# Kernel tuning notes

Hardware: AMD Instinct MI355X
Metric: run time of the kernel (lower is better)

## Reference

```python
import jax, jax.numpy as jnp
import numpy as np

U = I = 4096; E = 128; K = 4; D = E // K; R = 3; B = 512; L = 100
LAMB = 0.5; L2NORM = 1e-4; EPS = 1e-8


def _l2norm(x, axis):
    n = jnp.sqrt(jnp.sum(x * x, axis=axis, keepdims=True))
    return x / jnp.maximum(n, 1e-12)


def setup_inputs() -> dict:
    key = jax.random.key(0)
    ks = jax.random.split(key, 16)
    def adj(k, shape, p=0.01):
        return jax.random.bernoulli(k, p, shape).astype(jnp.float32)
    relation_mats = adj(ks[0], (R, U, I))
    item_graphs = adj(ks[1], (R, I, I))
    train_matrix = relation_mats[0]
    inp = {
        "user": jax.random.randint(ks[2], (B, 1), 0, U),
        "item": jax.random.randint(ks[3], (B, L), 0, I),
        "user_embedding": jax.random.normal(ks[4], (U, E), jnp.float32) * 0.1,
        "item_embedding": jax.random.normal(ks[5], (I, E), jnp.float32) * 0.1,
        "mgnn_weight": jax.random.normal(ks[6], (R,), jnp.float32),
        "item_behaviour_W": jax.random.normal(ks[7], (R, E, E), jnp.float32) * 0.05,
        "item_propagate_W": jax.random.normal(ks[8], (R, E, E), jnp.float32) * 0.05,
        "W": jax.random.normal(ks[9], (E, E), jnp.float32) * 0.05,
        "W_K": jax.random.normal(ks[10], (K, D, E), jnp.float32) * 0.05,
        "B_K": jax.random.normal(ks[11], (K, D), jnp.float32) * 0.05,
        "train_matrix": train_matrix,
        "relation_mats": relation_mats,
        "item_graphs": item_graphs,
        "item_graph_degree": item_graphs.sum(axis=2, keepdims=True),  # [R,I,1]
        "user_behaviour_degree": relation_mats.sum(axis=2).T,  # [U,R]
    }
    return inp


def reference(user, item, user_embedding, item_embedding, mgnn_weight,
              item_behaviour_W, item_propagate_W, W, W_K, B_K,
              train_matrix, relation_mats, item_graphs, item_graph_degree,
              user_behaviour_degree):
    # behaviour weighting: [U,R]
    total_weight = user_behaviour_degree @ mgnn_weight[:, None]  # [U,1]
    ubw = user_behaviour_degree * mgnn_weight[None, :] / (total_weight + EPS)

    # K-head projections (relation-independent; original recomputes identically per relation)
    s_i = _l2norm(jax.nn.relu(jnp.einsum('kde,ie->kdi', W_K, item_embedding) + B_K[..., None]), axis=1)  # [K,D,I]
    s_u0 = _l2norm(jax.nn.relu(jnp.einsum('kde,ue->kdu', W_K, user_embedding) + B_K[..., None]), axis=1)  # [K,D,U]
    s_u0 = jnp.transpose(s_u0, (2, 0, 1))  # [U,K,D]

    ue_blocks = user_embedding.reshape(U, K, D)
    logits = jnp.einsum('ukd,kdi->kui', ue_blocks, s_i)  # [K,U,I]
    r = jax.nn.softmax(logits, axis=0)  # exp / sum over K heads

    user_feature = jnp.zeros((U, E), user_embedding.dtype)
    score2 = jnp.zeros((B, L), user_embedding.dtype)
    for i in range(R):
        rel = relation_mats[i]  # [U,I]
        # item-item propagation
        tip = ((item_graphs[i] @ item_embedding) / (item_graph_degree[i] + EPS)) @ item_propagate_W[i]  # [I,E]
        tmp_item_emb = tip[item]  # [B,L,E]
        # attention-weighted user-item propagation per head
        s_u = s_u0 + jnp.einsum('kui,kdi->ukd', r * rel[None], s_i)  # [U,K,D]
        tun = _l2norm(s_u, axis=2).reshape(U, E)  # tmp_user_neighbour
        tuinp = (rel @ tip) / (user_behaviour_degree[:, i:i + 1] + EPS)  # [U,E]
        user_feature = user_feature + ubw[:, i:i + 1] * tun
        proj = tuinp @ item_behaviour_W[i]  # [U,E]
        score2 = score2 + jnp.sum(proj[user[:, 0]][:, None, :] * tmp_item_emb, axis=2)
    score2 = score2 / R

    item_feature = (train_matrix.T @ user_embedding) @ W  # [I,E]
    user_feature = user_feature @ W  # [U,E]

    uf = user_feature[user[:, 0]][:, None, :]  # [B,1,E]
    itf = item_feature[item]  # [B,L,E]
    score1 = jnp.sum(uf * itf, axis=2)  # [B,L]
    scores = score1 + LAMB * score2
    L2_loss = L2NORM * (L * jnp.sum(uf ** 2) + jnp.sum(itf ** 2))
    return scores, L2_loss
```

## Files before the change

### kernel.cpp

```cpp
#include <hip/hip_runtime.h>

#define NU 4096
#define NI 4096
#define NR 3
#define NB 512
#define NL 100
#define FEPS 1e-8f

typedef float nf4 __attribute__((ext_vector_type(4)));

#define WS_SI    0
#define WS_EMBW  524288
#define WS_TIP   2097152
#define WS_UEW   3670016
#define WS_ITEMF 4194304
#define WS_PROJ  4915200
#define WS_UF    5111808
#define WS_UF2P  5177344
#define WS_ITF2P 5177856
#define WS_BMT   5190656

__global__ void k_prep(const float* __restrict__ iemb, const float* __restrict__ ipW,
                       const float* __restrict__ uemb, const float* __restrict__ Wm,
                       const float* __restrict__ WK, const float* __restrict__ BK,
                       const float* __restrict__ tm,
                       float* __restrict__ embW, float* __restrict__ uew,
                       float* __restrict__ si, unsigned long long* __restrict__ bmT) {
  int t = threadIdx.x;
  int bid = blockIdx.x;
  if (bid < 4096) {
    __shared__ unsigned char nib[4][256];
    const nf4* r4 = (const nf4*)(tm + (size_t)bid * NI);
#pragma unroll
    for (int q = 0; q < 4; ++q) {
      nf4 v = __builtin_nontemporal_load(&r4[q * 256 + t]);
      unsigned m = 0;
      if (v.x != 0.f) m |= 1u;
      if (v.y != 0.f) m |= 2u;
      if (v.z != 0.f) m |= 4u;
      if (v.w != 0.f) m |= 8u;
      nib[q][t] = (unsigned char)m;
    }
    __syncthreads();
    if (t < 64) {
      unsigned long long mm = 0;
#pragma unroll
      for (int j = 0; j < 16; ++j) {
        int e = t * 16 + j;
        mm |= (unsigned long long)nib[e >> 8][e & 255] << (4 * j);
      }
      bmT[(size_t)t * NU + bid] = mm;
    }
  } else if (bid < 5120) {
    __shared__ __align__(16) float shbuf[2048];
    int lb = bid - 4096;
    int batch = lb >> 8, rb = lb & 255;
    const float* in;
    const float* Wp;
    float* out;
    if (batch < 3) {
      in = iemb;
      Wp = ipW + (size_t)batch * 16384;
      out = embW + (size_t)batch * NI * 128;
    } else {
      in = uemb; Wp = Wm; out = uew;
    }
    const float4* in4 = (const float4*)(in + (size_t)rb * 2048);
    for (int c = t; c < 512; c += 256) ((float4*)shbuf)[c] = in4[c];
    __syncthreads();
    int c = t & 127, g = t >> 7;
    float acc[8];
#pragma unroll
    for (int rr = 0; rr < 8; ++rr) acc[rr] = 0.f;
    for (int e = 0; e < 128; ++e) {
      float wv = Wp[e * 128 + c];
#pragma unroll
      for (int rr = 0; rr < 8; ++rr) acc[rr] += shbuf[(g * 8 + rr) * 128 + e] * wv;
    }
#pragma unroll
    for (int rr = 0; rr < 8; ++rr) out[((size_t)rb * 16 + g * 8 + rr) * 128 + c] = acc[rr];
  } else {
    __shared__ __align__(16) float embs2[256];
    int tl = t & 127, half = t >> 7;
    int item = (bid - 5120) * 2 + half;
    float* embs = embs2 + half * 128;
    if (tl < 32) ((float4*)embs)[tl] = ((const float4*)(iemb + (size_t)item * 128))[tl];
    __syncthreads();
    float acc = BK[tl];
    const float4* wk4 = (const float4*)(WK + (size_t)tl * 128);
    const float4* e4 = (const float4*)embs;
#pragma unroll 8
    for (int cc = 0; cc < 32; ++cc) {
      float4 w = wk4[cc], v = e4[cc];
      acc += w.x * v.x + w.y * v.y + w.z * v.z + w.w * v.w;
    }
    acc = fmaxf(acc, 0.f);
    float sq = acc * acc;
#pragma unroll
    for (int m = 1; m <= 16; m <<= 1) sq += __shfl_xor(sq, m);
    si[(size_t)item * 128 + tl] = acc / fmaxf(sqrtf(sq), 1e-12f);
  }
}

__global__ void k_tipf(const float* __restrict__ G, const float* __restrict__ deg,
                       const float* __restrict__ embW,
                       const unsigned long long* __restrict__ bmT,
                       const float* __restrict__ uew,
                       float* __restrict__ tip, float* __restrict__ itemf) {
  int t = threadIdx.x;
  int bid = blockIdx.x;
  if (bid < 12288) {
    int r = bid >> 12;
    const nf4* row4 = (const nf4*)(G + (size_t)bid * NI);
    __shared__ int nz[512];
    __shared__ int cnt;
    __shared__ float4 red[8][32];
    if (t == 0) cnt = 0;
    __syncthreads();
#pragma unroll
    for (int c = 0; c < 4; ++c) {
      int idx4 = c * 256 + t;
      nf4 v = __builtin_nontemporal_load(&row4[idx4]);
      int j0 = idx4 << 2;
      if (v.x != 0.f) nz[atomicAdd(&cnt, 1)] = j0;
      if (v.y != 0.f) nz[atomicAdd(&cnt, 1)] = j0 + 1;
      if (v.z != 0.f) nz[atomicAdd(&cnt, 1)] = j0 + 2;
      if (v.w != 0.f) nz[atomicAdd(&cnt, 1)] = j0 + 3;
    }
    __syncthreads();
    int n = min(cnt, 512);
    int g = t >> 5, f = t & 31;
    float4 acc = {0.f, 0.f, 0.f, 0.f};
    const float4* e4 = (const float4*)(embW + (size_t)r * NI * 128);
    for (int p = g; p < n; p += 8) {
      float4 v = e4[(size_t)nz[p] * 32 + f];
      acc.x += v.x; acc.y += v.y; acc.z += v.z; acc.w += v.w;
    }
    red[g][f] = acc;
    __syncthreads();
    if (t < 32) {
      float4 s = red[0][t];
#pragma unroll
      for (int q = 1; q < 8; ++q) {
        float4 v = red[q][t];
        s.x += v.x; s.y += v.y; s.z += v.z; s.w += v.w;
      }
      float inv = 1.f / (deg[bid] + FEPS);
      s.x *= inv; s.y *= inv; s.z *= inv; s.w *= inv;
      ((float4*)(tip + (size_t)bid * 128))[t] = s;
    }
  } else {
    int i = bid - 12288;
    int ct = i >> 6;
    unsigned long long bitm = 1ull << (i & 63);
    __shared__ int lst[192];
    __shared__ int cnt2;
    __shared__ float red2[3][128];
    if (t == 0) cnt2 = 0;
    __syncthreads();
    const unsigned long long* col = bmT + (size_t)ct * NU;
#pragma unroll
    for (int cc = 0; cc < 16; ++cc) {
      unsigned long long m = col[cc * 256 + t];
      if (m & bitm) lst[atomicAdd(&cnt2, 1)] = cc * 256 + t;
    }
    __syncthreads();
    int n = min(cnt2, 192);
    int w = t >> 6, l = t & 63;
    float ax = 0.f, ay = 0.f;
    const float2* uew2 = (const float2*)uew;
    for (int p = w; p < n; p += 4) {
      float2 v = uew2[(size_t)lst[p] * 64 + l];
      ax += v.x; ay += v.y;
    }
    if (w > 0) { red2[w - 1][2 * l] = ax; red2[w - 1][2 * l + 1] = ay; }
    __syncthreads();
    if (w == 0) {
      float2 o;
      o.x = ax + red2[0][2 * l] + red2[1][2 * l] + red2[2][2 * l];
      o.y = ay + red2[0][2 * l + 1] + red2[1][2 * l + 1] + red2[2][2 * l + 1];
      ((float2*)(itemf + (size_t)i * 128))[l] = o;
    }
  }
}

__global__ void k_user2(const int* __restrict__ user, const float* __restrict__ relm,
                        const float* __restrict__ si, const float* __restrict__ tip,
                        const float* __restrict__ uemb, const float* __restrict__ WK,
                        const float* __restrict__ BK, const float* __restrict__ ibW,
                        const float* __restrict__ ubd, const float* __restrict__ mw,
                        const float* __restrict__ Wm,
                        float* __restrict__ proj, float* __restrict__ uf,
                        float* __restrict__ uf2p) {
  int b = blockIdx.x;
  int t = threadIdx.x;
  int u = user[b];
  __shared__ int nz[512];
  __shared__ int cnt;
  __shared__ __align__(16) float uel[128];
  __shared__ float su0[128];
  __shared__ float comb[128];
  __shared__ float tu[128];
  __shared__ float redA[4][128];
  __shared__ float redB[4][128];
  __shared__ float part[2];
  if (t < 32) ((float4*)uel)[t] = ((const float4*)(uemb + (size_t)u * 128))[t];
  __syncthreads();
  if (t < 128) {
    float a = BK[t];
    const float4* wk4 = (const float4*)(WK + (size_t)t * 128);
    const float4* ue4 = (const float4*)uel;
#pragma unroll 8
    for (int c = 0; c < 32; ++c) {
      float4 w = wk4[c], v = ue4[c];
      a += w.x * v.x + w.y * v.y + w.z * v.z + w.w * v.w;
    }
    a = fmaxf(a, 0.f);
    float sq = a * a;
#pragma unroll
    for (int m = 1; m <= 16; m <<= 1) sq += __shfl_xor(sq, m);
    su0[t] = a / fmaxf(sqrtf(sq), 1e-12f);
    comb[t] = 0.f;
  }
  float d0 = ubd[u * 3], d1 = ubd[u * 3 + 1], d2 = ubd[u * 3 + 2];
  float w0 = mw[0], w1 = mw[1], w2 = mw[2];
  float tw = d0 * w0 + d1 * w1 + d2 * w2;
  int wid = t >> 6, lane = t & 63;
  int k = lane >> 4;
  const float2* si2 = (const float2*)si;
  for (int r = 0; r < 3; ++r) {
    if (t == 0) cnt = 0;
    __syncthreads();
    const nf4* rel4 = (const nf4*)(relm + ((size_t)r * NU + u) * NI);
#pragma unroll
    for (int c = 0; c < 4; ++c) {
      int idx4 = c * 256 + t;
      nf4 v = __builtin_nontemporal_load(&rel4[idx4]);
      int j0 = idx4 << 2;
      if (v.x != 0.f) nz[atomicAdd(&cnt, 1)] = j0;
      if (v.y != 0.f) nz[atomicAdd(&cnt, 1)] = j0 + 1;
      if (v.z != 0.f) nz[atomicAdd(&cnt, 1)] = j0 + 2;
      if (v.w != 0.f) nz[atomicAdd(&cnt, 1)] = j0 + 3;
    }
    __syncthreads();
    int n = min(cnt, 512);
    float2 myue = ((const float2*)uel)[lane];
    float sux = 0.f, suy = 0.f, tpx = 0.f, tpy = 0.f;
    const float2* tip2 = (const float2*)(tip + (size_t)r * NI * 128);
    for (int p = wid; p < n; p += 4) {
      int i = nz[p];
      float2 sv = si2[(size_t)i * 64 + lane];
      float lg = myue.x * sv.x + myue.y * sv.y;
      lg += __shfl_xor(lg, 1);
      lg += __shfl_xor(lg, 2);
      lg += __shfl_xor(lg, 4);
      lg += __shfl_xor(lg, 8);
      float l0 = __shfl(lg, 0), l1 = __shfl(lg, 16), l2 = __shfl(lg, 32), l3 = __shfl(lg, 48);
      float mx = fmaxf(fmaxf(l0, l1), fmaxf(l2, l3));
      float e0 = __expf(l0 - mx), e1 = __expf(l1 - mx), e2 = __expf(l2 - mx), e3 = __expf(l3 - mx);
      float inv = 1.f / (e0 + e1 + e2 + e3);
      float myr = (k == 0 ? e0 : k == 1 ? e1 : k == 2 ? e2 : e3) * inv;
      sux += myr * sv.x;
      suy += myr * sv.y;
      float2 tv = tip2[(size_t)i * 64 + lane];
      tpx += tv.x;
      tpy += tv.y;
    }
    redA[wid][2 * lane] = sux; redA[wid][2 * lane + 1] = suy;
    redB[wid][2 * lane] = tpx; redB[wid][2 * lane + 1] = tpy;
    __syncthreads();
    if (t < 128) {
      float suv = redA[0][t] + redA[1][t] + redA[2][t] + redA[3][t];
      float tipv = redB[0][t] + redB[1][t] + redB[2][t] + redB[3][t];
      float su = su0[t] + suv;
      float sq2 = su * su;
#pragma unroll
      for (int m = 1; m <= 16; m <<= 1) sq2 += __shfl_xor(sq2, m);
      float tun = su / fmaxf(sqrtf(sq2), 1e-12f);
      float dr = (r == 0 ? d0 : r == 1 ? d1 : d2);
      float wr = (r == 0 ? w0 : r == 1 ? w1 : w2);
      comb[t] += (dr * wr / (tw + FEPS)) * tun;
      tu[t] = tipv / (dr + FEPS);
    }
    __syncthreads();
    int ep = t & 127, hh = t >> 7;
    const float* Wb = ibW + (size_t)r * 16384;
    float pacc = 0.f;
    for (int e = hh * 64; e < hh * 64 + 64; ++e) pacc += tu[e] * Wb[e * 128 + ep];
    redA[hh][ep] = pacc;
    __syncthreads();
    if (hh == 0) proj[(size_t)(b * 3 + r) * 128 + ep] = redA[0][ep] + redA[1][ep];
    __syncthreads();
  }
  if (t < 128) {
    float acc = 0.f;
    for (int e = 0; e < 128; ++e) acc += comb[e] * Wm[e * 128 + t];
    uf[(size_t)b * 128 + t] = acc;
    float sq = acc * acc;
#pragma unroll
    for (int m = 1; m <= 32; m <<= 1) sq += __shfl_xor(sq, m);
    if ((t & 63) == 0) part[t >> 6] = sq;
  }
  __syncthreads();
  if (t == 0) uf2p[b] = part[0] + part[1];
}

__global__ void k_score(const int* __restrict__ item, const float* __restrict__ itemf,
                        const float* __restrict__ uf, const float* __restrict__ tip,
                        const float* __restrict__ proj, float* __restrict__ out,
                        float* __restrict__ itf2p) {
  int t = threadIdx.x, wid = t >> 6, lane = t & 63;
  int idx = blockIdx.x * 4 + wid;
  int b = idx / NL;
  int it = item[idx];
  float2 av = ((const float2*)(itemf + (size_t)it * 128))[lane];
  float2 cv = ((const float2*)(uf + (size_t)b * 128))[lane];
  float s1 = av.x * cv.x + av.y * cv.y;
  float sqi = av.x * av.x + av.y * av.y;
  float s2 = 0.f;
#pragma unroll
  for (int r = 0; r < 3; ++r) {
    float2 tv = ((const float2*)(tip + ((size_t)r * NI + it) * 128))[lane];
    float2 pv = ((const float2*)(proj + (size_t)(b * 3 + r) * 128))[lane];
    s2 += tv.x * pv.x + tv.y * pv.y;
  }
#pragma unroll
  for (int m = 1; m <= 32; m <<= 1) {
    s1 += __shfl_xor(s1, m);
    s2 += __shfl_xor(s2, m);
    sqi += __shfl_xor(sqi, m);
  }
  if (lane == 0) out[idx] = s1 + 0.5f * (s2 * (1.f / 3.f));
  __shared__ float sh[4];
  if (lane == 0) sh[wid] = sqi;
  __syncthreads();
  if (t == 0) itf2p[blockIdx.x] = sh[0] + sh[1] + sh[2] + sh[3];
}

__global__ void k_final(const float* __restrict__ itf2p, const float* __restrict__ uf2p,
                        float* __restrict__ out) {
  int t = threadIdx.x;
  float v = 0.f;
  for (int i = t; i < 12800; i += 256) v += itf2p[i];
  float vu = 0.f;
  for (int i = t; i < NB; i += 256) vu += uf2p[i];
  v += 100.f * vu;
#pragma unroll
  for (int m = 1; m <= 32; m <<= 1) v += __shfl_xor(v, m);
  __shared__ float sh[4];
  if ((t & 63) == 0) sh[t >> 6] = v;
  __syncthreads();
  if (t == 0) out[NB * NL] = 1e-4f * (sh[0] + sh[1] + sh[2] + sh[3]);
}

extern "C" void kernel_launch(void* const* d_in, const int* in_sizes, int n_in,
                              void* d_out, int out_size, void* d_ws, size_t ws_size,
                              hipStream_t stream) {
  (void)in_sizes; (void)n_in; (void)out_size; (void)ws_size;
  const int* user = (const int*)d_in[0];
  const int* item = (const int*)d_in[1];
  const float* uemb = (const float*)d_in[2];
  const float* iemb = (const float*)d_in[3];
  const float* mw = (const float*)d_in[4];
  const float* ibW = (const float*)d_in[5];
  const float* ipW = (const float*)d_in[6];
  const float* Wm = (const float*)d_in[7];
  const float* WK = (const float*)d_in[8];
  const float* BK = (const float*)d_in[9];
  const float* tm = (const float*)d_in[10];
  const float* relm = (const float*)d_in[11];
  const float* ig = (const float*)d_in[12];
  const float* igd = (const float*)d_in[13];
  const float* ubd = (const float*)d_in[14];
  float* out = (float*)d_out;
  float* ws = (float*)d_ws;
  unsigned long long* bmT = (unsigned long long*)(ws + WS_BMT);

  k_prep<<<7168, 256, 0, stream>>>(iemb, ipW, uemb, Wm, WK, BK, tm,
                                   ws + WS_EMBW, ws + WS_UEW, ws + WS_SI, bmT);
  k_tipf<<<16384, 256, 0, stream>>>(ig, igd, ws + WS_EMBW, bmT, ws + WS_UEW,
                                    ws + WS_TIP, ws + WS_ITEMF);
  k_user2<<<NB, 256, 0, stream>>>(user, relm, ws + WS_SI, ws + WS_TIP, uemb, WK, BK,
                                  ibW, ubd, mw, Wm, ws + WS_PROJ, ws + WS_UF,
                                  ws + WS_UF2P);
  k_score<<<12800, 256, 0, stream>>>(item, ws + WS_ITEMF, ws + WS_UF, ws + WS_TIP,
                                     ws + WS_PROJ, out, ws + WS_ITF2P);
  k_final<<<1, 256, 0, stream>>>(ws + WS_ITF2P, ws + WS_UF2P, out);
}
```

Baseline: 205.2 us.

## Regroup kernels into scan/user stages and replace final reduction with atomics

Regroups the work into new stages. The train-matrix bitmask scan moves into the item-graph scan kernel, item-feature gathering is co-scheduled with the per-user kernel, and k_final is removed in favour of atomic accumulation of the L2 loss into the output. Each scan block now handles two item-graph rows with all loads issued up front, and nontemporal loads become plain loads. The aim is to cut launch count, improve load overlap, and let independent stages share the GPU. The cost is a float atomic reduction whose summation order is nondeterministic, plus a zero-initialisation that relies on stream ordering.

```diff
diff --git a/kernel.cpp b/kernel.cpp
--- a/kernel.cpp
+++ b/kernel.cpp
@@ -6,8 +6,6 @@
 #define NB 512
 #define NL 100
 #define FEPS 1e-8f
-
-typedef float nf4 __attribute__((ext_vector_type(4)));
 
 #define WS_SI    0
 #define WS_EMBW  524288
@@ -16,54 +14,28 @@
 #define WS_ITEMF 4194304
 #define WS_PROJ  4915200
 #define WS_UF    5111808
-#define WS_UF2P  5177344
-#define WS_ITF2P 5177856
 #define WS_BMT   5190656
 
-__global__ void k_prep(const float* __restrict__ iemb, const float* __restrict__ ipW,
-                       const float* __restrict__ uemb, const float* __restrict__ Wm,
-                       const float* __restrict__ WK, const float* __restrict__ BK,
-                       const float* __restrict__ tm,
-                       float* __restrict__ embW, float* __restrict__ uew,
-                       float* __restrict__ si, unsigned long long* __restrict__ bmT) {
+__global__ void k_bmm_si(const float* __restrict__ iemb, const float* __restrict__ ipW,
+                         const float* __restrict__ uemb, const float* __restrict__ Wm,
+                         const float* __restrict__ WK, const float* __restrict__ BK,
+                         float* __restrict__ embW, float* __restrict__ uew,
+                         float* __restrict__ si, float* __restrict__ out) {
   int t = threadIdx.x;
   int bid = blockIdx.x;
-  if (bid < 4096) {
-    __shared__ unsigned char nib[4][256];
-    const nf4* r4 = (const nf4*)(tm + (size_t)bid * NI);
-#pragma unroll
-    for (int q = 0; q < 4; ++q) {
-      nf4 v = __builtin_nontemporal_load(&r4[q * 256 + t]);
-      unsigned m = 0;
-      if (v.x != 0.f) m |= 1u;
-      if (v.y != 0.f) m |= 2u;
-      if (v.z != 0.f) m |= 4u;
-      if (v.w != 0.f) m |= 8u;
-      nib[q][t] = (unsigned char)m;
-    }
-    __syncthreads();
-    if (t < 64) {
-      unsigned long long mm = 0;
-#pragma unroll
-      for (int j = 0; j < 16; ++j) {
-        int e = t * 16 + j;
-        mm |= (unsigned long long)nib[e >> 8][e & 255] << (4 * j);
-      }
-      bmT[(size_t)t * NU + bid] = mm;
-    }
-  } else if (bid < 5120) {
+  if (bid == 0 && t == 0) out[NB * NL] = 0.f;
+  if (bid < 1024) {
     __shared__ __align__(16) float shbuf[2048];
-    int lb = bid - 4096;
-    int batch = lb >> 8, rb = lb & 255;
+    int batch = bid >> 8, rb = bid & 255;
     const float* in;
     const float* Wp;
-    float* out;
+    float* outp;
     if (batch < 3) {
       in = iemb;
       Wp = ipW + (size_t)batch * 16384;
-      out = embW + (size_t)batch * NI * 128;
+      outp = embW + (size_t)batch * NI * 128;
     } else {
-      in = uemb; Wp = Wm; out = uew;
+      in = uemb; Wp = Wm; outp = uew;
     }
     const float4* in4 = (const float4*)(in + (size_t)rb * 2048);
     for (int c = t; c < 512; c += 256) ((float4*)shbuf)[c] = in4[c];
@@ -78,11 +50,11 @@
       for (int rr = 0; rr < 8; ++rr) acc[rr] += shbuf[(g * 8 + rr) * 128 + e] * wv;
     }
 #pragma unroll
-    for (int rr = 0; rr < 8; ++rr) out[((size_t)rb * 16 + g * 8 + rr) * 128 + c] = acc[rr];
+    for (int rr = 0; rr < 8; ++rr) outp[((size_t)rb * 16 + g * 8 + rr) * 128 + c] = acc[rr];
   } else {
     __shared__ __align__(16) float embs2[256];
     int tl = t & 127, half = t >> 7;
-    int item = (bid - 5120) * 2 + half;
+    int item = (bid - 1024) * 2 + half;
     float* embs = embs2 + half * 128;
     if (tl < 32) ((float4*)embs)[tl] = ((const float4*)(iemb + (size_t)item * 128))[tl];
     __syncthreads();
@@ -102,55 +74,129 @@
   }
 }
 
-__global__ void k_tipf(const float* __restrict__ G, const float* __restrict__ deg,
-                       const float* __restrict__ embW,
-                       const unsigned long long* __restrict__ bmT,
-                       const float* __restrict__ uew,
-                       float* __restrict__ tip, float* __restrict__ itemf) {
+__global__ void k_scan(const float* __restrict__ tm, const float* __restrict__ G,
+                       const float* __restrict__ deg, const float* __restrict__ embW,
+                       unsigned long long* __restrict__ bmT, float* __restrict__ tip) {
   int t = threadIdx.x;
   int bid = blockIdx.x;
-  if (bid < 12288) {
-    int r = bid >> 12;
-    const nf4* row4 = (const nf4*)(G + (size_t)bid * NI);
-    __shared__ int nz[512];
-    __shared__ int cnt;
+  if (bid < 4096) {
+    __shared__ unsigned char nib[4][256];
+    const float4* r4 = (const float4*)(tm + (size_t)bid * NI);
+    float4 v0 = r4[t], v1 = r4[256 + t], v2 = r4[512 + t], v3 = r4[768 + t];
+#pragma unroll
+    for (int q = 0; q < 4; ++q) {
+      float4 v = (q == 0) ? v0 : (q == 1) ? v1 : (q == 2) ? v2 : v3;
+      unsigned m = 0;
+      if (v.x != 0.f) m |= 1u;
+      if (v.y != 0.f) m |= 2u;
+      if (v.z != 0.f) m |= 4u;
+      if (v.w != 0.f) m |= 8u;
+      nib[q][t] = (unsigned char)m;
+    }
+    __syncthreads();
+    if (t < 64) {
+      unsigned long long mm = 0;
+#pragma unroll
+      for (int j = 0; j < 16; ++j) {
+        int e = t * 16 + j;
+        mm |= (unsigned long long)nib[e >> 8][e & 255] << (4 * j);
+      }
+      bmT[(size_t)t * NU + bid] = mm;
+    }
+  } else {
+    int gid0 = (bid - 4096) * 2;
+    __shared__ int nzA[512], nzB[512];
+    __shared__ int cntA, cntB;
     __shared__ float4 red[8][32];
-    if (t == 0) cnt = 0;
-    __syncthreads();
+    if (t == 0) { cntA = 0; cntB = 0; }
+    __syncthreads();
+    const float4* rowA = (const float4*)(G + (size_t)gid0 * NI);
+    const float4* rowB = (const float4*)(G + (size_t)(gid0 + 1) * NI);
+    float4 a0 = rowA[t], a1 = rowA[256 + t], a2 = rowA[512 + t], a3 = rowA[768 + t];
+    float4 b0 = rowB[t], b1 = rowB[256 + t], b2 = rowB[512 + t], b3 = rowB[768 + t];
 #pragma unroll
     for (int c = 0; c < 4; ++c) {
-      int idx4 = c * 256 + t;
-      nf4 v = __builtin_nontemporal_load(&row4[idx4]);
-      int j0 = idx4 << 2;
-      if (v.x != 0.f) nz[atomicAdd(&cnt, 1)] = j0;
-      if (v.y != 0.f) nz[atomicAdd(&cnt, 1)] = j0 + 1;
-      if (v.z != 0.f) nz[atomicAdd(&cnt, 1)] = j0 + 2;
-      if (v.w != 0.f) nz[atomicAdd(&cnt, 1)] = j0 + 3;
-    }
-    __syncthreads();
-    int n = min(cnt, 512);
+      float4 v = (c == 0) ? a0 : (c == 1) ? a1 : (c == 2) ? a2 : a3;
+      int j0 = (c * 256 + t) << 2;
+      if (v.x != 0.f) nzA[atomicAdd(&cntA, 1)] = j0;
+      if (v.y != 0.f) nzA[atomicAdd(&cntA, 1)] = j0 + 1;
+      if (v.z != 0.f) nzA[atomicAdd(&cntA, 1)] = j0 + 2;
+      if (v.w != 0.f) nzA[atomicAdd(&cntA, 1)] = j0 + 3;
+    }
+#pragma unroll
+    for (int c = 0; c < 4; ++c) {
+      float4 v = (c == 0) ? b0 : (c == 1) ? b1 : (c == 2) ? b2 : b3;
+      int j0 = (c * 256 + t) << 2;
+      if (v.x != 0.f) nzB[atomicAdd(&cntB, 1)] = j0;
+      if (v.y != 0.f) nzB[atomicAdd(&cntB, 1)] = j0 + 1;
+      if (v.z != 0.f) nzB[atomicAdd(&cntB, 1)] = j0 + 2;
+      if (v.w != 0.f) nzB[atomicAdd(&cntB, 1)] = j0 + 3;
+    }
+    __syncthreads();
     int g = t >> 5, f = t & 31;
-    float4 acc = {0.f, 0.f, 0.f, 0.f};
-    const float4* e4 = (const float4*)(embW + (size_t)r * NI * 128);
-    for (int p = g; p < n; p += 8) {
-      float4 v = e4[(size_t)nz[p] * 32 + f];
-      acc.x += v.x; acc.y += v.y; acc.z += v.z; acc.w += v.w;
-    }
-    red[g][f] = acc;
-    __syncthreads();
-    if (t < 32) {
-      float4 s = red[0][t];
-#pragma unroll
-      for (int q = 1; q < 8; ++q) {
-        float4 v = red[q][t];
-        s.x += v.x; s.y += v.y; s.z += v.z; s.w += v.w;
-      }
-      float inv = 1.f / (deg[bid] + FEPS);
-      s.x *= inv; s.y *= inv; s.z *= inv; s.w *= inv;
-      ((float4*)(tip + (size_t)bid * 128))[t] = s;
-    }
-  } else {
-    int i = bid - 12288;
+    {
+      int r = gid0 >> 12;
+      int n = min(cntA, 512);
+      float4 acc = {0.f, 0.f, 0.f, 0.f};
+      const float4* e4 = (const float4*)(embW + (size_t)r * NI * 128);
+      for (int p = g; p < n; p += 8) {
+        float4 v = e4[(size_t)nzA[p] * 32 + f];
+        acc.x += v.x; acc.y += v.y; acc.z += v.z; acc.w += v.w;
+      }
+      red[g][f] = acc;
+      __syncthreads();
+      if (t < 32) {
+        float4 s = red[0][t];
+#pragma unroll
+        for (int q = 1; q < 8; ++q) {
+          float4 v = red[q][t];
+          s.x += v.x; s.y += v.y; s.z += v.z; s.w += v.w;
+        }
+        float inv = 1.f / (deg[gid0] + FEPS);
+        s.x *= inv; s.y *= inv; s.z *= inv; s.w *= inv;
+        ((float4*)(tip + (size_t)gid0 * 128))[t] = s;
+      }
+      __syncthreads();
+    }
+    {
+      int r = (gid0 + 1) >> 12;
+      int n = min(cntB, 512);
+      float4 acc = {0.f, 0.f, 0.f, 0.f};
+      const float4* e4 = (const float4*)(embW + (size_t)r * NI * 128);
+      for (int p = g; p < n; p += 8) {
+        float4 v = e4[(size_t)nzB[p] * 32 + f];
+        acc.x += v.x; acc.y += v.y; acc.z += v.z; acc.w += v.w;
+      }
+      red[g][f] = acc;
+      __syncthreads();
+      if (t < 32) {
+        float4 s = red[0][t];
+#pragma unroll
+        for (int q = 1; q < 8; ++q) {
+          float4 v = red[q][t];
+          s.x += v.x; s.y += v.y; s.z += v.z; s.w += v.w;
+        }
+        float inv = 1.f / (deg[gid0 + 1] + FEPS);
+        s.x *= inv; s.y *= inv; s.z *= inv; s.w *= inv;
+        ((float4*)(tip + (size_t)(gid0 + 1) * 128))[t] = s;
+      }
+    }
+  }
+}
+
+__global__ void k_userf(const unsigned long long* __restrict__ bmT,
+                        const float* __restrict__ uew, float* __restrict__ itemf,
+                        const int* __restrict__ user, const float* __restrict__ relm,
+                        const float* __restrict__ si, const float* __restrict__ tip,
+                        const float* __restrict__ uemb, const float* __restrict__ WK,
+                        const float* __restrict__ BK, const float* __restrict__ ibW,
+                        const float* __restrict__ ubd, const float* __restrict__ mw,
+                        const float* __restrict__ Wm, float* __restrict__ proj,
+                        float* __restrict__ uf, float* __restrict__ out) {
+  int t = threadIdx.x;
+  int bid = blockIdx.x;
+  if (bid < 4096) {
+    int i = bid;
     int ct = i >> 6;
     unsigned long long bitm = 1ull << (i & 63);
     __shared__ int lst[192];
@@ -181,134 +227,123 @@
       o.y = ay + red2[0][2 * l + 1] + red2[1][2 * l + 1] + red2[2][2 * l + 1];
       ((float2*)(itemf + (size_t)i * 128))[l] = o;
     }
+  } else {
+    int b = bid - 4096;
+    int u = user[b];
+    __shared__ int nz[512];
+    __shared__ int cnt;
+    __shared__ __align__(16) float uel[128];
+    __shared__ float su0[128];
+    __shared__ float comb[128];
+    __shared__ float tu[128];
+    __shared__ float redA[4][128];
+    __shared__ float redB[4][128];
+    __shared__ float part[2];
+    if (t < 32) ((float4*)uel)[t] = ((const float4*)(uemb + (size_t)u * 128))[t];
+    __syncthreads();
+    if (t < 128) {
+      float a = BK[t];
+      const float4* wk4 = (const float4*)(WK + (size_t)t * 128);
+      const float4* ue4 = (const float4*)uel;
+#pragma unroll 8
+      for (int c = 0; c < 32; ++c) {
+        float4 w = wk4[c], v = ue4[c];
+        a += w.x * v.x + w.y * v.y + w.z * v.z + w.w * v.w;
+      }
+      a = fmaxf(a, 0.f);
+      float sq = a * a;
+#pragma unroll
+      for (int m = 1; m <= 16; m <<= 1) sq += __shfl_xor(sq, m);
+      su0[t] = a / fmaxf(sqrtf(sq), 1e-12f);
+      comb[t] = 0.f;
+    }
+    float d0 = ubd[u * 3], d1 = ubd[u * 3 + 1], d2 = ubd[u * 3 + 2];
+    float w0 = mw[0], w1 = mw[1], w2 = mw[2];
+    float tw = d0 * w0 + d1 * w1 + d2 * w2;
+    int wid = t >> 6, lane = t & 63;
+    int k = lane >> 4;
+    const float2* si2 = (const float2*)si;
+    for (int r = 0; r < 3; ++r) {
+      if (t == 0) cnt = 0;
+      __syncthreads();
+      const float4* rel4 = (const float4*)(relm + ((size_t)r * NU + u) * NI);
+      float4 q0 = rel4[t], q1 = rel4[256 + t], q2 = rel4[512 + t], q3 = rel4[768 + t];
+#pragma unroll
+      for (int c = 0; c < 4; ++c) {
+        float4 v = (c == 0) ? q0 : (c == 1) ? q1 : (c == 2) ? q2 : q3;
+        int j0 = (c * 256 + t) << 2;
+        if (v.x != 0.f) nz[atomicAdd(&cnt, 1)] = j0;
+        if (v.y != 0.f) nz[atomicAdd(&cnt, 1)] = j0 + 1;
+        if (v.z != 0.f) nz[atomicAdd(&cnt, 1)] = j0 + 2;
+        if (v.w != 0.f) nz[atomicAdd(&cnt, 1)] = j0 + 3;
+      }
+      __syncthreads();
+      int n = min(cnt, 512);
+      float2 myue = ((const float2*)uel)[lane];
+      float sux = 0.f, suy = 0.f, tpx = 0.f, tpy = 0.f;
+      const float2* tip2 = (const float2*)(tip + (size_t)r * NI * 128);
+      for (int p = wid; p < n; p += 4) {
+        int i = nz[p];
+        float2 sv = si2[(size_t)i * 64 + lane];
+        float lg = myue.x * sv.x + myue.y * sv.y;
+        lg += __shfl_xor(lg, 1);
+        lg += __shfl_xor(lg, 2);
+        lg += __shfl_xor(lg, 4);
+        lg += __shfl_xor(lg, 8);
+        float l0 = __shfl(lg, 0), l1 = __shfl(lg, 16), l2 = __shfl(lg, 32), l3 = __shfl(lg, 48);
+        float mx = fmaxf(fmaxf(l0, l1), fmaxf(l2, l3));
+        float e0 = __expf(l0 - mx), e1 = __expf(l1 - mx), e2 = __expf(l2 - mx), e3 = __expf(l3 - mx);
+        float inv = 1.f / (e0 + e1 + e2 + e3);
+        float myr = (k == 0 ? e0 : k == 1 ? e1 : k == 2 ? e2 : e3) * inv;
+        sux += myr * sv.x;
+        suy += myr * sv.y;
+        float2 tv = tip2[(size_t)i * 64 + lane];
+        tpx += tv.x;
+        tpy += tv.y;
+      }
+      redA[wid][2 * lane] = sux; redA[wid][2 * lane + 1] = suy;
+      redB[wid][2 * lane] = tpx; redB[wid][2 * lane + 1] = tpy;
+      __syncthreads();
+      if (t < 128) {
+        float suv = redA[0][t] + redA[1][t] + redA[2][t] + redA[3][t];
+        float tipv = redB[0][t] + redB[1][t] + redB[2][t] + redB[3][t];
+        float su = su0[t] + suv;
+        float sq2 = su * su;
+#pragma unroll
+        for (int m = 1; m <= 16; m <<= 1) sq2 += __shfl_xor(sq2, m);
+        float tun = su / fmaxf(sqrtf(sq2), 1e-12f);
+        float dr = (r == 0 ? d0 : r == 1 ? d1 : d2);
+        float wr = (r == 0 ? w0 : r == 1 ? w1 : w2);
+        comb[t] += (dr * wr / (tw + FEPS)) * tun;
+        tu[t] = tipv / (dr + FEPS);
+      }
+      __syncthreads();
+      int ep = t & 127, hh = t >> 7;
+      const float* Wb = ibW + (size_t)r * 16384;
+      float pacc = 0.f;
+      for (int e = hh * 64; e < hh * 64 + 64; ++e) pacc += tu[e] * Wb[e * 128 + ep];
+      redA[hh][ep] = pacc;
+      __syncthreads();
+      if (hh == 0) proj[(size_t)(b * 3 + r) * 128 + ep] = redA[0][ep] + redA[1][ep];
+      __syncthreads();
+    }
+    if (t < 128) {
+      float acc = 0.f;
+      for (int e = 0; e < 128; ++e) acc += comb[e] * Wm[e * 128 + t];
+      uf[(size_t)b * 128 + t] = acc;
+      float sq = acc * acc;
+#pragma unroll
+      for (int m = 1; m <= 32; m <<= 1) sq += __shfl_xor(sq, m);
+      if ((t & 63) == 0) part[t >> 6] = sq;
+    }
+    __syncthreads();
+    if (t == 0) atomicAdd(&out[NB * NL], 0.01f * (part[0] + part[1]));
   }
 }
 
-__global__ void k_user2(const int* __restrict__ user, const float* __restrict__ relm,
-                        const float* __restrict__ si, const float* __restrict__ tip,
-                        const float* __restrict__ uemb, const float* __restrict__ WK,
-                        const float* __restrict__ BK, const float* __restrict__ ibW,
-                        const float* __restrict__ ubd, const float* __restrict__ mw,
-                        const float* __restrict__ Wm,
-                        float* __restrict__ proj, float* __restrict__ uf,
-                        float* __restrict__ uf2p) {
-  int b = blockIdx.x;
-  int t = threadIdx.x;
-  int u = user[b];
-  __shared__ int nz[512];
-  __shared__ int cnt;
-  __shared__ __align__(16) float uel[128];
-  __shared__ float su0[128];
-  __shared__ float comb[128];
-  __shared__ float tu[128];
-  __shared__ float redA[4][128];
-  __shared__ float redB[4][128];
-  __shared__ float part[2];
-  if (t < 32) ((float4*)uel)[t] = ((const float4*)(uemb + (size_t)u * 128))[t];
-  __syncthreads();
-  if (t < 128) {
-    float a = BK[t];
-    const float4* wk4 = (const float4*)(WK + (size_t)t * 128);
-    const float4* ue4 = (const float4*)uel;
-#pragma unroll 8
-    for (int c = 0; c < 32; ++c) {
-      float4 w = wk4[c], v = ue4[c];
-      a += w.x * v.x + w.y * v.y + w.z * v.z + w.w * v.w;
-    }
-    a = fmaxf(a, 0.f);
-    float sq = a * a;
-#pragma unroll
-    for (int m = 1; m <= 16; m <<= 1) sq += __shfl_xor(sq, m);
-    su0[t] = a / fmaxf(sqrtf(sq), 1e-12f);
-    comb[t] = 0.f;
-  }
-  float d0 = ubd[u * 3], d1 = ubd[u * 3 + 1], d2 = ubd[u * 3 + 2];
-  float w0 = mw[0], w1 = mw[1], w2 = mw[2];
-  float tw = d0 * w0 + d1 * w1 + d2 * w2;
-  int wid = t >> 6, lane = t & 63;
-  int k = lane >> 4;
-  const float2* si2 = (const float2*)si;
-  for (int r = 0; r < 3; ++r) {
-    if (t == 0) cnt = 0;
-    __syncthreads();
-    const nf4* rel4 = (const nf4*)(relm + ((size_t)r * NU + u) * NI);
-#pragma unroll
-    for (int c = 0; c < 4; ++c) {
-      int idx4 = c * 256 + t;
-      nf4 v = __builtin_nontemporal_load(&rel4[idx4]);
-      int j0 = idx4 << 2;
-      if (v.x != 0.f) nz[atomicAdd(&cnt, 1)] = j0;
-      if (v.y != 0.f) nz[atomicAdd(&cnt, 1)] = j0 + 1;
-      if (v.z != 0.f) nz[atomicAdd(&cnt, 1)] = j0 + 2;
-      if (v.w != 0.f) nz[atomicAdd(&cnt, 1)] = j0 + 3;
-    }
-    __syncthreads();
-    int n = min(cnt, 512);
-    float2 myue = ((const float2*)uel)[lane];
-    float sux = 0.f, suy = 0.f, tpx = 0.f, tpy = 0.f;
-    const float2* tip2 = (const float2*)(tip + (size_t)r * NI * 128);
-    for (int p = wid; p < n; p += 4) {
-      int i = nz[p];
-      float2 sv = si2[(size_t)i * 64 + lane];
-      float lg = myue.x * sv.x + myue.y * sv.y;
-      lg += __shfl_xor(lg, 1);
-      lg += __shfl_xor(lg, 2);
-      lg += __shfl_xor(lg, 4);
-      lg += __shfl_xor(lg, 8);
-      float l0 = __shfl(lg, 0), l1 = __shfl(lg, 16), l2 = __shfl(lg, 32), l3 = __shfl(lg, 48);
-      float mx = fmaxf(fmaxf(l0, l1), fmaxf(l2, l3));
-      float e0 = __expf(l0 - mx), e1 = __expf(l1 - mx), e2 = __expf(l2 - mx), e3 = __expf(l3 - mx);
-      float inv = 1.f / (e0 + e1 + e2 + e3);
-      float myr = (k == 0 ? e0 : k == 1 ? e1 : k == 2 ? e2 : e3) * inv;
-      sux += myr * sv.x;
-      suy += myr * sv.y;
-      float2 tv = tip2[(size_t)i * 64 + lane];
-      tpx += tv.x;
-      tpy += tv.y;
-    }
-    redA[wid][2 * lane] = sux; redA[wid][2 * lane + 1] = suy;
-    redB[wid][2 * lane] = tpx; redB[wid][2 * lane + 1] = tpy;
-    __syncthreads();
-    if (t < 128) {
-      float suv = redA[0][t] + redA[1][t] + redA[2][t] + redA[3][t];
-      float tipv = redB[0][t] + redB[1][t] + redB[2][t] + redB[3][t];
-      float su = su0[t] + suv;
-      float sq2 = su * su;
-#pragma unroll
-      for (int m = 1; m <= 16; m <<= 1) sq2 += __shfl_xor(sq2, m);
-      float tun = su / fmaxf(sqrtf(sq2), 1e-12f);
-      float dr = (r == 0 ? d0 : r == 1 ? d1 : d2);
-      float wr = (r == 0 ? w0 : r == 1 ? w1 : w2);
-      comb[t] += (dr * wr / (tw + FEPS)) * tun;
-      tu[t] = tipv / (dr + FEPS);
-    }
-    __syncthreads();
-    int ep = t & 127, hh = t >> 7;
-    const float* Wb = ibW + (size_t)r * 16384;
-    float pacc = 0.f;
-    for (int e = hh * 64; e < hh * 64 + 64; ++e) pacc += tu[e] * Wb[e * 128 + ep];
-    redA[hh][ep] = pacc;
-    __syncthreads();
-    if (hh == 0) proj[(size_t)(b * 3 + r) * 128 + ep] = redA[0][ep] + redA[1][ep];
-    __syncthreads();
-  }
-  if (t < 128) {
-    float acc = 0.f;
-    for (int e = 0; e < 128; ++e) acc += comb[e] * Wm[e * 128 + t];
-    uf[(size_t)b * 128 + t] = acc;
-    float sq = acc * acc;
-#pragma unroll
-    for (int m = 1; m <= 32; m <<= 1) sq += __shfl_xor(sq, m);
-    if ((t & 63) == 0) part[t >> 6] = sq;
-  }
-  __syncthreads();
-  if (t == 0) uf2p[b] = part[0] + part[1];
-}
-
 __global__ void k_score(const int* __restrict__ item, const float* __restrict__ itemf,
                         const float* __restrict__ uf, const float* __restrict__ tip,
-                        const float* __restrict__ proj, float* __restrict__ out,
-                        float* __restrict__ itf2p) {
+                        const float* __restrict__ proj, float* __restrict__ out) {
   int t = threadIdx.x, wid = t >> 6, lane = t & 63;
   int idx = blockIdx.x * 4 + wid;
   int b = idx / NL;
@@ -334,23 +369,7 @@
   __shared__ float sh[4];
   if (lane == 0) sh[wid] = sqi;
   __syncthreads();
-  if (t == 0) itf2p[blockIdx.x] = sh[0] + sh[1] + sh[2] + sh[3];
-}
-
-__global__ void k_final(const float* __restrict__ itf2p, const float* __restrict__ uf2p,
-                        float* __restrict__ out) {
-  int t = threadIdx.x;
-  float v = 0.f;
-  for (int i = t; i < 12800; i += 256) v += itf2p[i];
-  float vu = 0.f;
-  for (int i = t; i < NB; i += 256) vu += uf2p[i];
-  v += 100.f * vu;
-#pragma unroll
-  for (int m = 1; m <= 32; m <<= 1) v += __shfl_xor(v, m);
-  __shared__ float sh[4];
-  if ((t & 63) == 0) sh[t >> 6] = v;
-  __syncthreads();
-  if (t == 0) out[NB * NL] = 1e-4f * (sh[0] + sh[1] + sh[2] + sh[3]);
+  if (t == 0) atomicAdd(&out[NB * NL], 1e-4f * (sh[0] + sh[1] + sh[2] + sh[3]));
 }
 
 extern "C" void kernel_launch(void* const* d_in, const int* in_sizes, int n_in,
@@ -376,14 +395,12 @@
   float* ws = (float*)d_ws;
   unsigned long long* bmT = (unsigned long long*)(ws + WS_BMT);
 
-  k_prep<<<7168, 256, 0, stream>>>(iemb, ipW, uemb, Wm, WK, BK, tm,
-                                   ws + WS_EMBW, ws + WS_UEW, ws + WS_SI, bmT);
-  k_tipf<<<16384, 256, 0, stream>>>(ig, igd, ws + WS_EMBW, bmT, ws + WS_UEW,
-                                    ws + WS_TIP, ws + WS_ITEMF);
-  k_user2<<<NB, 256, 0, stream>>>(user, relm, ws + WS_SI, ws + WS_TIP, uemb, WK, BK,
-                                  ibW, ubd, mw, Wm, ws + WS_PROJ, ws + WS_UF,
-                                  ws + WS_UF2P);
+  k_bmm_si<<<3072, 256, 0, stream>>>(iemb, ipW, uemb, Wm, WK, BK,
+                                     ws + WS_EMBW, ws + WS_UEW, ws + WS_SI, out);
+  k_scan<<<10240, 256, 0, stream>>>(tm, ig, igd, ws + WS_EMBW, bmT, ws + WS_TIP);
+  k_userf<<<4608, 256, 0, stream>>>(bmT, ws + WS_UEW, ws + WS_ITEMF, user, relm,
+                                    ws + WS_SI, ws + WS_TIP, uemb, WK, BK, ibW,
+                                    ubd, mw, Wm, ws + WS_PROJ, ws + WS_UF, out);
   k_score<<<12800, 256, 0, stream>>>(item, ws + WS_ITEMF, ws + WS_UF, ws + WS_TIP,
-                                     ws + WS_PROJ, out, ws + WS_ITF2P);
-  k_final<<<1, 256, 0, stream>>>(ws + WS_ITF2P, ws + WS_UF2P, out);
+                                     ws + WS_PROJ, out);
 }
```

Result: slower. 354.9 us (+72.9%).
